# Kernel optimization log

Measured on AMD Instinct MI355X. Metric: run time of the kernel, lower is better.

## Reference

```python
import jax, jax.numpy as jnp
import numpy as np

B, S, D_MODEL, N_HEADS, MAX_LEN = 2, 1024, 1024, 16, 1024
D_K = D_MODEL // N_HEADS


def setup_inputs() -> dict:
    key = jax.random.key(0)
    ks = jax.random.split(key, 8)
    w_std = 1.0 / np.sqrt(D_MODEL)  # ~ torch Linear default scale
    inp = {
        "query": jax.random.normal(ks[0], (B, S, D_MODEL), jnp.float32),
        "key": jax.random.normal(ks[1], (B, S, D_MODEL), jnp.float32),
        "value": jax.random.normal(ks[2], (B, S, D_MODEL), jnp.float32),
        "Wq": jax.random.normal(ks[3], (D_MODEL, D_MODEL), jnp.float32) * w_std,
        "Wk": jax.random.normal(ks[4], (D_MODEL, D_MODEL), jnp.float32) * w_std,
        "Wv": jax.random.normal(ks[5], (D_MODEL, D_MODEL), jnp.float32) * w_std,
        "Wo": jax.random.normal(ks[6], (D_MODEL, D_MODEL), jnp.float32) * w_std,
        "bq": jnp.zeros((D_MODEL,), jnp.float32),
        "bk": jnp.zeros((D_MODEL,), jnp.float32),
        "bv": jnp.zeros((D_MODEL,), jnp.float32),
        "bo": jnp.zeros((D_MODEL,), jnp.float32),
        "Er": jax.random.normal(ks[7], (2 * MAX_LEN - 1, D_K), jnp.float32) * 0.02,
    }
    return inp


def _rel_positions(q_len, k_len, max_len):
    pos = jnp.arange(q_len)[:, None] - jnp.arange(k_len)[None, :]
    pos = jnp.clip(pos, -max_len + 1, max_len - 1)
    return pos + max_len - 1  # [q_len, k_len] indices into Er


def reference(query, key, value, Wq, Wk, Wv, Wo, bq, bk, bv, bo, Er):
    b, q_len, d_model = query.shape
    k_len = key.shape[1]
    d_k = Er.shape[-1]
    h = d_model // d_k
    scale = 1.0 / np.sqrt(d_k)

    def proj(x, W, bias):  # torch Linear: x @ W.T + b, then split heads -> [b,h,s,d_k]
        y = x @ W.T + bias
        return y.reshape(b, -1, h, d_k).transpose(0, 2, 1, 3)

    q = proj(query, Wq, bq)
    k = proj(key, Wk, bk)
    v = proj(value, Wv, bv)

    positions = _rel_positions(q_len, k_len, MAX_LEN)  # [q,k]
    # QEr[b,h,q,k] = sum_d q[b,h,q,d] * Er[positions[q,k], d]
    # computed as a full contraction against Er then a gather on the relative axis
    qe_all = jnp.einsum('bhqd,rd->bhqr', q, Er)  # [b,h,q,2*max_len-1]
    qer = jnp.take_along_axis(qe_all, positions[None, None, :, :], axis=-1)  # [b,h,q,k]

    qk = jnp.einsum('bhqd,bhkd->bhqk', q, k)
    scores = (qk + qer) * scale
    p_attn = jax.nn.softmax(scores, axis=-1)  # dropout=0.0 (eval)
    out = jnp.einsum('bhqk,bhkd->bhqd', p_attn, v)

    out = out.transpose(0, 2, 1, 3).reshape(b, q_len, h * d_k)
    return out @ Wo.T + bo
```

## Files before the change

kernel.cpp:

```cpp
#include <hip/hip_runtime.h>
#include <hip/hip_bf16.h>
#include <cstdint>
#include <cstddef>

typedef __attribute__((ext_vector_type(8))) short bf16x8;
typedef __attribute__((ext_vector_type(4))) float f32x4;
typedef unsigned short u16;
typedef unsigned int u32;

#define DEV static __device__ __forceinline__

constexpr int Sc = 1024, DMc = 1024, Hc = 16, DKc = 64;

DEV u16 f2bf(float f) {
  u32 u = __float_as_uint(f);
  return (u16)((u + 0x7FFFu + ((u >> 16) & 1u)) >> 16);
}
DEV float bf2f(u16 h) { return __uint_as_float(((u32)h) << 16); }

#define GLDS16(g, l)                                                        \
  __builtin_amdgcn_global_load_lds(                                         \
      (const __attribute__((address_space(1))) void*)(g),                   \
      (__attribute__((address_space(3))) void*)(l), 16, 0, 0)

struct CvtJob { const float* in; u16* out; int nchunk; int rsh; int nreal; };
struct CvtArgs { CvtJob j[8]; };

__global__ __launch_bounds__(256) void cvt_kernel(CvtArgs a) {
  CvtJob job = a.j[blockIdx.y];
  int ci = (int)(blockIdx.x * 256 + threadIdx.x);
  if (ci >= job.nchunk) return;
  bf16x8 o = {};
  if (ci < job.nreal) {
    const float* src = job.in + (size_t)ci * 8;
    float4 v0 = *(const float4*)src;
    float4 v1 = *(const float4*)(src + 4);
    o[0] = (short)f2bf(v0.x); o[1] = (short)f2bf(v0.y);
    o[2] = (short)f2bf(v0.z); o[3] = (short)f2bf(v0.w);
    o[4] = (short)f2bf(v1.x); o[5] = (short)f2bf(v1.y);
    o[6] = (short)f2bf(v1.z); o[7] = (short)f2bf(v1.w);
  }
  int row = ci >> job.rsh;
  int co = (ci & ~7) | ((ci & 7) ^ (row & 7));
  *(bf16x8*)(job.out + (size_t)co * 8) = o;
}

struct GemmJob { const u16* A; const u16* W; const float* bias; void* out; };
struct GemmArgs { GemmJob p[3]; };

template<int BM, int MODE>
__global__ __launch_bounds__(256, 2) void gemm_bt(GemmArgs G) {
  constexpr int MI = BM / 32;
  __shared__ __align__(16) u16 sA[2][BM * 64];
  __shared__ __align__(16) u16 sB[2][128 * 64];
  const int tid = threadIdx.x, lane = tid & 63, w = tid >> 6;
  const int cl = lane & 15, rg = lane >> 4;
  const int srow = lane >> 3, schk = lane & 7;
  int z, m0, n0;
  if (MODE == 0) {
    int id = blockIdx.x;
    if (id < 512) { z = id >> 8; int r = id & 255; m0 = (r >> 3) * 64; n0 = (r & 7) * 128; }
    else          { z = 2;       int r = id - 512; m0 = (r >> 4) * 64; n0 = (r & 15) * 128; }
  } else {
    z = 0; int id = blockIdx.x; m0 = (id >> 3) * 64; n0 = (id & 7) * 128;
  }
  GemmJob P = G.p[z];
  constexpr int K = 1024;
  const int wm = (w >> 1) * (MI * 16), wn = (w & 1) * 64;
  f32x4 acc[MI][4] = {};

  auto stage = [&](int kt, int b) {
    const u16* Ab = P.A + (size_t)m0 * K + kt * 64;
    const u16* Wb = P.W + (size_t)n0 * K + kt * 64;
    #pragma unroll
    for (int i = 0; i < BM / 32; ++i)
      GLDS16(Ab + (size_t)(i * 32 + w * 8 + srow) * K + schk * 8, &sA[b][(i * 32 + w * 8) * 64]);
    #pragma unroll
    for (int i = 0; i < 4; ++i)
      GLDS16(Wb + (size_t)(i * 32 + w * 8 + srow) * K + schk * 8, &sB[b][(i * 32 + w * 8) * 64]);
  };

  stage(0, 0);
  for (int kt = 0; kt < 16; ++kt) {
    __syncthreads();
    if (kt < 15) stage(kt + 1, (kt + 1) & 1);
    const u16* A_ = sA[kt & 1];
    const u16* B_ = sB[kt & 1];
    #pragma unroll
    for (int kk = 0; kk < 2; ++kk) {
      bf16x8 af[MI], bfr[4];
      #pragma unroll
      for (int mi = 0; mi < MI; ++mi) {
        int row = wm + mi * 16 + cl;
        af[mi] = *(const bf16x8*)(A_ + row * 64 + ((kk * 4 + rg) ^ (row & 7)) * 8);
      }
      #pragma unroll
      for (int ni = 0; ni < 4; ++ni) {
        int row = wn + ni * 16 + cl;
        bfr[ni] = *(const bf16x8*)(B_ + row * 64 + ((kk * 4 + rg) ^ (row & 7)) * 8);
      }
      #pragma unroll
      for (int mi = 0; mi < MI; ++mi)
        #pragma unroll
        for (int ni = 0; ni < 4; ++ni)
          acc[mi][ni] = __builtin_amdgcn_mfma_f32_16x16x32_bf16(af[mi], bfr[ni], acc[mi][ni], 0, 0, 0);
    }
  }
  #pragma unroll
  for (int mi = 0; mi < MI; ++mi) {
    #pragma unroll
    for (int ni = 0; ni < 4; ++ni) {
      #pragma unroll
      for (int j = 0; j < 4; ++j) {
        int m = m0 + wm + mi * 16 + rg * 4 + j;
        int n = n0 + wn + ni * 16 + cl;
        if (MODE == 1) {
          ((float*)P.out)[(size_t)m * DMc + n] = acc[mi][ni][j] + P.bias[n];
        } else if (z < 2) {
          float v = acc[mi][ni][j] + P.bias[n];
          int h = n >> 6, d = n & 63;
          int c2 = (d >> 3) ^ (m & 7);
          ((u16*)P.out)[((size_t)((m >> 10) * Hc + h) * Sc + (m & 1023)) * DKc + c2 * 8 + (d & 7)] = f2bf(v);
        } else {
          float v = acc[mi][ni][j] + P.bias[m];
          int d = m & 63, h = m >> 6, bb = n >> 10, s = n & 1023;
          int c2 = ((s & 63) >> 3) ^ (d & 7);
          ((u16*)P.out)[((size_t)(bb * Hc + h) * DKc + d) * Sc + (s & ~63) + c2 * 8 + (s & 7)] = f2bf(v);
        }
      }
    }
  }
}

__global__ __launch_bounds__(256, 4) void attn_rel(
    const u16* __restrict__ qg, const u16* __restrict__ kg,
    const u16* __restrict__ vtg, const u16* __restrict__ erg,
    u16* __restrict__ Opart, float* __restrict__ lpart) {
  __shared__ __align__(16) u16 sK[64 * 64];
  __shared__ __align__(16) u16 sV[64 * 64];
  __shared__ __align__(16) u16 sU[4][1440];
  const int tid = threadIdx.x, lane = tid & 63, w = tid >> 6;
  const int cl = lane & 15, rg = lane >> 4;
  const int key = cl & 7;
  const int bh = blockIdx.x & 31, qt = (blockIdx.x >> 5) & 15, half = blockIdx.x >> 9;
  const int q0 = qt * 64, t0 = half * 8;

  const u16* qrow = qg + ((size_t)bh * Sc + q0 + w * 16 + cl) * DKc;
  bf16x8 qf0 = *(const bf16x8*)(qrow + (rg ^ key) * 8);
  bf16x8 qf1 = *(const bf16x8*)(qrow + ((rg + 4) ^ key) * 8);
  f32x4 oacc[4] = {};
  float lsum = 0.f;
  u16* Uw = sU[w];
  const u16* kbase = kg + (size_t)bh * Sc * DKc;
  const u16* vbase = vtg + (size_t)bh * DKc * Sc;

  auto stage = [&](int t) {
    const u16* ks = kbase + t * 64 * 64;
    #pragma unroll
    for (int i = 0; i < 2; ++i) {
      GLDS16(ks + (i * 32 + w * 8) * 64 + lane * 8, &sK[(i * 32 + w * 8) * 64]);
      GLDS16(vbase + (size_t)(i * 32 + w * 8 + (lane >> 3)) * Sc + t * 64 + (lane & 7) * 8,
             &sV[(i * 32 + w * 8) * 64]);
    }
  };

  stage(t0);
  for (int tt = 0; tt < 8; ++tt) {
    const int t = t0 + tt;
    __syncthreads();

    f32x4 sct[4];
    #pragma unroll
    for (int nc = 0; nc < 4; ++nc) {
      const u16* kr = sK + (nc * 16 + cl) * 64;
      bf16x8 b0 = *(const bf16x8*)(kr + (rg ^ key) * 8);
      bf16x8 b1 = *(const bf16x8*)(kr + ((rg + 4) ^ key) * 8);
      f32x4 a = {};
      a = __builtin_amdgcn_mfma_f32_16x16x32_bf16(b0, qf0, a, 0, 0, 0);
      a = __builtin_amdgcn_mfma_f32_16x16x32_bf16(b1, qf1, a, 0, 0, 0);
      sct[nc] = a;
    }
    const u16* ebase = erg + (size_t)(q0 + w * 16 - t * 64 + 960) * DKc;
    #pragma unroll
    for (int rc0 = 0; rc0 < 5; ++rc0) {
      const u16* er = ebase + (size_t)(rc0 * 16 + cl) * DKc;
      bf16x8 e0 = *(const bf16x8*)(er + (rg ^ key) * 8);
      bf16x8 e1 = *(const bf16x8*)(er + ((rg + 4) ^ key) * 8);
      f32x4 a = {};
      a = __builtin_amdgcn_mfma_f32_16x16x32_bf16(qf0, e0, a, 0, 0, 0);
      a = __builtin_amdgcn_mfma_f32_16x16x32_bf16(qf1, e1, a, 0, 0, 0);
      u16* tp = Uw + (rc0 * 16 + cl) * 18 + rg * 4;
      ushort2 lo, hi;
      lo.x = f2bf(a[0]); lo.y = f2bf(a[1]);
      hi.x = f2bf(a[2]); hi.y = f2bf(a[3]);
      *(ushort2*)tp = lo;
      *(ushort2*)(tp + 2) = hi;
    }
    float pv[4][4];
    #pragma unroll
    for (int nc = 0; nc < 4; ++nc) {
      #pragma unroll
      for (int j = 0; j < 4; ++j) {
        int r = cl + 63 - (nc * 16 + rg * 4 + j);
        float tval = bf2f(Uw[r * 18 + cl]);
        float p = __expf((sct[nc][j] + tval) * 0.125f);
        lsum += p;
        pv[nc][j] = p;
      }
    }
    #pragma unroll
    for (int nc = 0; nc < 4; ++nc) {
      ushort4 pk;
      pk.x = f2bf(pv[nc][0]); pk.y = f2bf(pv[nc][1]);
      pk.z = f2bf(pv[nc][2]); pk.w = f2bf(pv[nc][3]);
      *(ushort4*)(Uw + cl * 76 + nc * 16 + rg * 4) = pk;
    }
    bf16x8 pa0 = *(const bf16x8*)(Uw + cl * 76 + rg * 8);
    bf16x8 pa1 = *(const bf16x8*)(Uw + cl * 76 + 32 + rg * 8);
    #pragma unroll
    for (int dc = 0; dc < 4; ++dc) {
      const u16* vr = sV + (dc * 16 + cl) * 64;
      bf16x8 b0 = *(const bf16x8*)(vr + (rg ^ key) * 8);
      bf16x8 b1 = *(const bf16x8*)(vr + ((rg + 4) ^ key) * 8);
      oacc[dc] = __builtin_amdgcn_mfma_f32_16x16x32_bf16(pa0, b0, oacc[dc], 0, 0, 0);
      oacc[dc] = __builtin_amdgcn_mfma_f32_16x16x32_bf16(pa1, b1, oacc[dc], 0, 0, 0);
    }
    __syncthreads();
    if (tt < 7) stage(t + 1);
  }
  lsum += __shfl_xor(lsum, 16);
  lsum += __shfl_xor(lsum, 32);
  const size_t pb = (size_t)(half * 32 + bh) * Sc;
  if (rg == 0) lpart[pb + q0 + w * 16 + cl] = lsum;
  u16* Ob = Opart + (pb + q0 + w * 16) * DKc;
  #pragma unroll
  for (int dc = 0; dc < 4; ++dc)
    #pragma unroll
    for (int j = 0; j < 4; ++j)
      Ob[(rg * 4 + j) * DKc + dc * 16 + cl] = f2bf(oacc[dc][j]);
}

__global__ __launch_bounds__(256) void merge_kernel(
    const u16* __restrict__ O, const float* __restrict__ l,
    u16* __restrict__ attnb) {
  int ci = (int)(blockIdx.x * 256 + threadIdx.x);
  int bh = ci >> 13, rem = ci & 8191, s = rem >> 3, dc = rem & 7;
  const u16* o0 = O + ((size_t)bh * Sc + s) * DKc + dc * 8;
  const u16* o1 = o0 + (size_t)32 * Sc * DKc;
  float rinv = 1.0f / (l[(size_t)bh * Sc + s] + l[(size_t)(32 + bh) * Sc + s]);
  bf16x8 a = *(const bf16x8*)o0;
  bf16x8 b = *(const bf16x8*)o1;
  bf16x8 o;
  #pragma unroll
  for (int e = 0; e < 8; ++e)
    o[e] = (short)f2bf((bf2f((u16)a[e]) + bf2f((u16)b[e])) * rinv);
  int bb = bh >> 4, h = bh & 15;
  int c2 = dc ^ (s & 7);
  *(bf16x8*)(attnb + ((size_t)(bb * Sc + s)) * DMc + h * DKc + c2 * 8) = o;
}

extern "C" void kernel_launch(void* const* d_in, const int* in_sizes, int n_in,
                              void* d_out, int out_size, void* d_ws, size_t ws_size,
                              hipStream_t stream) {
  (void)in_sizes; (void)n_in; (void)out_size; (void)ws_size;
  const float* query = (const float*)d_in[0];
  const float* key_  = (const float*)d_in[1];
  const float* value = (const float*)d_in[2];
  const float* Wq = (const float*)d_in[3];
  const float* Wk = (const float*)d_in[4];
  const float* Wv = (const float*)d_in[5];
  const float* Wo = (const float*)d_in[6];
  const float* bq = (const float*)d_in[7];
  const float* bk = (const float*)d_in[8];
  const float* bv = (const float*)d_in[9];
  const float* bo = (const float*)d_in[10];
  const float* Er = (const float*)d_in[11];

  char* p = (char*)d_ws;
  size_t off = 0;
  auto alloc = [&](size_t bytes) {
    char* r = p + off;
    off += (bytes + 255) & ~(size_t)255;
    return r;
  };
  u16* Xq  = (u16*)alloc((size_t)2048 * 1024 * 2);
  u16* Xk  = (u16*)alloc((size_t)2048 * 1024 * 2);
  u16* Xv  = (u16*)alloc((size_t)2048 * 1024 * 2);
  u16* Wqb = (u16*)alloc((size_t)1024 * 1024 * 2);
  u16* Wkb = (u16*)alloc((size_t)1024 * 1024 * 2);
  u16* Wvb = (u16*)alloc((size_t)1024 * 1024 * 2);
  u16* Wob = (u16*)alloc((size_t)1024 * 1024 * 2);
  u16* Erb = (u16*)alloc((size_t)2048 * 64 * 2);
  u16* qh  = (u16*)alloc((size_t)2048 * 1024 * 2);
  u16* kh  = (u16*)alloc((size_t)2048 * 1024 * 2);
  u16* vt  = (u16*)alloc((size_t)2048 * 1024 * 2);
  u16* attnb = (u16*)alloc((size_t)2048 * 1024 * 2);
  u16* Opart = (u16*)alloc((size_t)2 * 32 * 1024 * 64 * 2);
  float* lpart = (float*)alloc((size_t)2 * 32 * 1024 * 4);

  CvtArgs ca;
  ca.j[0] = {query, Xq, 262144, 7, 262144};
  ca.j[1] = {key_,  Xk, 262144, 7, 262144};
  ca.j[2] = {value, Xv, 262144, 7, 262144};
  ca.j[3] = {Wq, Wqb, 131072, 7, 131072};
  ca.j[4] = {Wk, Wkb, 131072, 7, 131072};
  ca.j[5] = {Wv, Wvb, 131072, 7, 131072};
  ca.j[6] = {Wo, Wob, 131072, 7, 131072};
  ca.j[7] = {Er, Erb, 16384, 3, 16376};
  cvt_kernel<<<dim3(1024, 8, 1), 256, 0, stream>>>(ca);

  GemmArgs gp;
  gp.p[0] = {Xq, Wqb, bq, (void*)qh};
  gp.p[1] = {Xk, Wkb, bk, (void*)kh};
  gp.p[2] = {Wvb, Xv, bv, (void*)vt};
  gemm_bt<64, 0><<<dim3(768, 1, 1), 256, 0, stream>>>(gp);

  attn_rel<<<dim3(1024, 1, 1), 256, 0, stream>>>(qh, kh, vt, Erb, Opart, lpart);

  merge_kernel<<<dim3(1024, 1, 1), 256, 0, stream>>>(Opart, lpart, attnb);

  GemmArgs go;
  go.p[0] = {attnb, Wob, bo, d_out};
  go.p[1] = go.p[0];
  go.p[2] = go.p[0];
  gemm_bt<64, 1><<<dim3(256, 1, 1), 256, 0, stream>>>(go);
}
```

Baseline: 96.20 us.

## Fuse activation fp32-to-bf16 conversion and split-merge into GEMM operand loading

```diff
diff --git a/kernel.cpp b/kernel.cpp
--- a/kernel.cpp
+++ b/kernel.cpp
@@ -18,13 +18,19 @@
 }
 DEV float bf2f(u16 h) { return __uint_as_float(((u32)h) << 16); }
 
+DEV u32 cvtpk(float a, float b) {
+  u32 r;
+  asm("v_cvt_pk_bf16_f32 %0, %1, %2" : "=v"(r) : "v"(a), "v"(b));
+  return r;
+}
+
 #define GLDS16(g, l)                                                        \
   __builtin_amdgcn_global_load_lds(                                         \
       (const __attribute__((address_space(1))) void*)(g),                   \
       (__attribute__((address_space(3))) void*)(l), 16, 0, 0)
 
 struct CvtJob { const float* in; u16* out; int nchunk; int rsh; int nreal; };
-struct CvtArgs { CvtJob j[8]; };
+struct CvtArgs { CvtJob j[5]; };
 
 __global__ __launch_bounds__(256) void cvt_kernel(CvtArgs a) {
   CvtJob job = a.j[blockIdx.y];
@@ -45,78 +51,136 @@
   *(bf16x8*)(job.out + (size_t)co * 8) = o;
 }
 
-struct GemmJob { const u16* A; const u16* W; const float* bias; void* out; };
-struct GemmArgs { GemmJob p[3]; };
-
-template<int BM, int MODE>
+struct GemmJob { const void* A; const void* W; const float* bias; void* out; const float* aux; };
+struct GemmArgs { GemmJob p[2]; };
+
+template<int BM, int BN, int MODE>
 __global__ __launch_bounds__(256, 2) void gemm_bt(GemmArgs G) {
-  constexpr int MI = BM / 32;
+  constexpr int MI = BM / 32, NI = BN / 32;
   __shared__ __align__(16) u16 sA[2][BM * 64];
-  __shared__ __align__(16) u16 sB[2][128 * 64];
+  __shared__ __align__(16) u16 sB[2][BN * 64];
   const int tid = threadIdx.x, lane = tid & 63, w = tid >> 6;
   const int cl = lane & 15, rg = lane >> 4;
   const int srow = lane >> 3, schk = lane & 7;
   int z, m0, n0;
-  if (MODE == 0) {
-    int id = blockIdx.x;
-    if (id < 512) { z = id >> 8; int r = id & 255; m0 = (r >> 3) * 64; n0 = (r & 7) * 128; }
-    else          { z = 2;       int r = id - 512; m0 = (r >> 4) * 64; n0 = (r & 15) * 128; }
-  } else {
-    z = 0; int id = blockIdx.x; m0 = (id >> 3) * 64; n0 = (id & 7) * 128;
-  }
+  if (MODE == 0)      { int id = blockIdx.x; z = id >> 8; int r = id & 255; m0 = (r >> 3) * 64; n0 = (r & 7) * 128; }
+  else if (MODE == 2) { int id = blockIdx.x; z = 0; m0 = (id >> 5) * 64; n0 = (id & 31) * 64; }
+  else                { int id = blockIdx.x; z = 0; m0 = (id >> 4) * 64; n0 = (id & 15) * 64; }
   GemmJob P = G.p[z];
-  constexpr int K = 1024;
-  const int wm = (w >> 1) * (MI * 16), wn = (w & 1) * 64;
-  f32x4 acc[MI][4] = {};
-
-  auto stage = [&](int kt, int b) {
-    const u16* Ab = P.A + (size_t)m0 * K + kt * 64;
-    const u16* Wb = P.W + (size_t)n0 * K + kt * 64;
-    #pragma unroll
-    for (int i = 0; i < BM / 32; ++i)
-      GLDS16(Ab + (size_t)(i * 32 + w * 8 + srow) * K + schk * 8, &sA[b][(i * 32 + w * 8) * 64]);
-    #pragma unroll
-    for (int i = 0; i < 4; ++i)
-      GLDS16(Wb + (size_t)(i * 32 + w * 8 + srow) * K + schk * 8, &sB[b][(i * 32 + w * 8) * 64]);
+  const int wm = (w >> 1) * (BM / 2), wn = (w & 1) * (BN / 2);
+  f32x4 acc[MI][NI] = {};
+
+  float4 fa[2][2];
+  bf16x8 ma[2][2];
+  float  ml[2][2];
+
+  auto issue = [&](int kt, int b) {
+    if (MODE == 0) {
+      #pragma unroll
+      for (int i = 0; i < 2; ++i) {
+        int ch = i * 256 + tid, row = ch >> 3, c = ch & 7;
+        const float* src = (const float*)P.A + (size_t)(m0 + row) * 1024 + kt * 64 + c * 8;
+        fa[i][0] = *(const float4*)src;
+        fa[i][1] = *(const float4*)(src + 4);
+      }
+      #pragma unroll
+      for (int i = 0; i < 4; ++i)
+        GLDS16((const u16*)P.W + (size_t)(n0 + i * 32 + w * 8 + srow) * 1024 + kt * 64 + schk * 8,
+               &sB[b][(i * 32 + w * 8) * 64]);
+    } else if (MODE == 2) {
+      #pragma unroll
+      for (int i = 0; i < 2; ++i) {
+        int ch = i * 256 + tid, row = ch >> 3, c = ch & 7;
+        const float* src = (const float*)P.W + (size_t)(n0 + row) * 1024 + kt * 64 + c * 8;
+        fa[i][0] = *(const float4*)src;
+        fa[i][1] = *(const float4*)(src + 4);
+      }
+      #pragma unroll
+      for (int i = 0; i < 2; ++i)
+        GLDS16((const u16*)P.A + (size_t)(m0 + i * 32 + w * 8 + srow) * 1024 + kt * 64 + schk * 8,
+               &sA[b][(i * 32 + w * 8) * 64]);
+    } else {
+      #pragma unroll
+      for (int i = 0; i < 2; ++i) {
+        int ch = i * 256 + tid, row = ch >> 3, c = ch & 7;
+        int rgl = m0 + row, bb = rgl >> 10, s = rgl & 1023;
+        const u16* o0 = (const u16*)P.A + ((size_t)(bb * 16 + kt) * 1024 + s) * 64 + c * 8;
+        ma[i][0] = *(const bf16x8*)o0;
+        ma[i][1] = *(const bf16x8*)(o0 + (size_t)32 * 1024 * 64);
+        ml[i][0] = P.aux[(size_t)(bb * 16 + kt) * 1024 + s];
+        ml[i][1] = P.aux[(size_t)(32 + bb * 16 + kt) * 1024 + s];
+      }
+      #pragma unroll
+      for (int i = 0; i < 2; ++i)
+        GLDS16((const u16*)P.W + (size_t)(n0 + i * 32 + w * 8 + srow) * 1024 + kt * 64 + schk * 8,
+               &sB[b][(i * 32 + w * 8) * 64]);
+    }
   };
 
-  stage(0, 0);
+  auto commit = [&](int b) {
+    #pragma unroll
+    for (int i = 0; i < 2; ++i) {
+      int ch = i * 256 + tid, row = ch >> 3, c = ch & 7;
+      uint4 v4;
+      if (MODE == 0 || MODE == 2) {
+        v4.x = cvtpk(fa[i][0].x, fa[i][0].y);
+        v4.y = cvtpk(fa[i][0].z, fa[i][0].w);
+        v4.z = cvtpk(fa[i][1].x, fa[i][1].y);
+        v4.w = cvtpk(fa[i][1].z, fa[i][1].w);
+      } else {
+        float rinv = 1.0f / (ml[i][0] + ml[i][1]);
+        u32 pk[4];
+        #pragma unroll
+        for (int p = 0; p < 4; ++p) {
+          float v0 = (bf2f((u16)ma[i][0][2 * p])     + bf2f((u16)ma[i][1][2 * p]))     * rinv;
+          float v1 = (bf2f((u16)ma[i][0][2 * p + 1]) + bf2f((u16)ma[i][1][2 * p + 1])) * rinv;
+          pk[p] = cvtpk(v0, v1);
+        }
+        v4.x = pk[0]; v4.y = pk[1]; v4.z = pk[2]; v4.w = pk[3];
+      }
+      u16* dst = (MODE == 2) ? sB[b] : sA[b];
+      *(uint4*)(dst + row * 64 + (c ^ (row & 7)) * 8) = v4;
+    }
+  };
+
+  issue(0, 0);
+  commit(0);
   for (int kt = 0; kt < 16; ++kt) {
     __syncthreads();
-    if (kt < 15) stage(kt + 1, (kt + 1) & 1);
-    const u16* A_ = sA[kt & 1];
-    const u16* B_ = sB[kt & 1];
+    const int b = kt & 1;
+    if (kt < 15) issue(kt + 1, b ^ 1);
     #pragma unroll
     for (int kk = 0; kk < 2; ++kk) {
-      bf16x8 af[MI], bfr[4];
+      bf16x8 af[MI], bfr[NI];
       #pragma unroll
       for (int mi = 0; mi < MI; ++mi) {
         int row = wm + mi * 16 + cl;
-        af[mi] = *(const bf16x8*)(A_ + row * 64 + ((kk * 4 + rg) ^ (row & 7)) * 8);
-      }
-      #pragma unroll
-      for (int ni = 0; ni < 4; ++ni) {
+        af[mi] = *(const bf16x8*)(sA[b] + row * 64 + ((kk * 4 + rg) ^ (row & 7)) * 8);
+      }
+      #pragma unroll
+      for (int ni = 0; ni < NI; ++ni) {
         int row = wn + ni * 16 + cl;
-        bfr[ni] = *(const bf16x8*)(B_ + row * 64 + ((kk * 4 + rg) ^ (row & 7)) * 8);
+        bfr[ni] = *(const bf16x8*)(sB[b] + row * 64 + ((kk * 4 + rg) ^ (row & 7)) * 8);
       }
       #pragma unroll
       for (int mi = 0; mi < MI; ++mi)
         #pragma unroll
-        for (int ni = 0; ni < 4; ++ni)
+        for (int ni = 0; ni < NI; ++ni)
           acc[mi][ni] = __builtin_amdgcn_mfma_f32_16x16x32_bf16(af[mi], bfr[ni], acc[mi][ni], 0, 0, 0);
     }
+    if (kt < 15) commit(b ^ 1);
   }
   #pragma unroll
   for (int mi = 0; mi < MI; ++mi) {
     #pragma unroll
-    for (int ni = 0; ni < 4; ++ni) {
+    for (int ni = 0; ni < NI; ++ni) {
       #pragma unroll
       for (int j = 0; j < 4; ++j) {
         int m = m0 + wm + mi * 16 + rg * 4 + j;
         int n = n0 + wn + ni * 16 + cl;
         if (MODE == 1) {
           ((float*)P.out)[(size_t)m * DMc + n] = acc[mi][ni][j] + P.bias[n];
-        } else if (z < 2) {
+        } else if (MODE == 0) {
           float v = acc[mi][ni][j] + P.bias[n];
           int h = n >> 6, d = n & 63;
           int c2 = (d >> 3) ^ (m & 7);
@@ -196,6 +260,8 @@
       *(ushort2*)tp = lo;
       *(ushort2*)(tp + 2) = hi;
     }
+    asm volatile("s_waitcnt lgkmcnt(0)" ::: "memory");
+    __builtin_amdgcn_sched_barrier(0);
     float pv[4][4];
     #pragma unroll
     for (int nc = 0; nc < 4; ++nc) {
@@ -215,6 +281,8 @@
       pk.z = f2bf(pv[nc][2]); pk.w = f2bf(pv[nc][3]);
       *(ushort4*)(Uw + cl * 76 + nc * 16 + rg * 4) = pk;
     }
+    asm volatile("s_waitcnt lgkmcnt(0)" ::: "memory");
+    __builtin_amdgcn_sched_barrier(0);
     bf16x8 pa0 = *(const bf16x8*)(Uw + cl * 76 + rg * 8);
     bf16x8 pa1 = *(const bf16x8*)(Uw + cl * 76 + 32 + rg * 8);
     #pragma unroll
@@ -238,25 +306,6 @@
     #pragma unroll
     for (int j = 0; j < 4; ++j)
       Ob[(rg * 4 + j) * DKc + dc * 16 + cl] = f2bf(oacc[dc][j]);
-}
-
-__global__ __launch_bounds__(256) void merge_kernel(
-    const u16* __restrict__ O, const float* __restrict__ l,
-    u16* __restrict__ attnb) {
-  int ci = (int)(blockIdx.x * 256 + threadIdx.x);
-  int bh = ci >> 13, rem = ci & 8191, s = rem >> 3, dc = rem & 7;
-  const u16* o0 = O + ((size_t)bh * Sc + s) * DKc + dc * 8;
-  const u16* o1 = o0 + (size_t)32 * Sc * DKc;
-  float rinv = 1.0f / (l[(size_t)bh * Sc + s] + l[(size_t)(32 + bh) * Sc + s]);
-  bf16x8 a = *(const bf16x8*)o0;
-  bf16x8 b = *(const bf16x8*)o1;
-  bf16x8 o;
-  #pragma unroll
-  for (int e = 0; e < 8; ++e)
-    o[e] = (short)f2bf((bf2f((u16)a[e]) + bf2f((u16)b[e])) * rinv);
-  int bb = bh >> 4, h = bh & 15;
-  int c2 = dc ^ (s & 7);
-  *(bf16x8*)(attnb + ((size_t)(bb * Sc + s)) * DMc + h * DKc + c2 * 8) = o;
 }
 
 extern "C" void kernel_launch(void* const* d_in, const int* in_sizes, int n_in,
@@ -283,9 +332,6 @@
     off += (bytes + 255) & ~(size_t)255;
     return r;
   };
-  u16* Xq  = (u16*)alloc((size_t)2048 * 1024 * 2);
-  u16* Xk  = (u16*)alloc((size_t)2048 * 1024 * 2);
-  u16* Xv  = (u16*)alloc((size_t)2048 * 1024 * 2);
   u16* Wqb = (u16*)alloc((size_t)1024 * 1024 * 2);
   u16* Wkb = (u16*)alloc((size_t)1024 * 1024 * 2);
   u16* Wvb = (u16*)alloc((size_t)1024 * 1024 * 2);
@@ -294,34 +340,31 @@
   u16* qh  = (u16*)alloc((size_t)2048 * 1024 * 2);
   u16* kh  = (u16*)alloc((size_t)2048 * 1024 * 2);
   u16* vt  = (u16*)alloc((size_t)2048 * 1024 * 2);
-  u16* attnb = (u16*)alloc((size_t)2048 * 1024 * 2);
   u16* Opart = (u16*)alloc((size_t)2 * 32 * 1024 * 64 * 2);
   float* lpart = (float*)alloc((size_t)2 * 32 * 1024 * 4);
 
   CvtArgs ca;
-  ca.j[0] = {query, Xq, 262144, 7, 262144};
-  ca.j[1] = {key_,  Xk, 262144, 7, 262144};
-  ca.j[2] = {value, Xv, 262144, 7, 262144};
-  ca.j[3] = {Wq, Wqb, 131072, 7, 131072};
-  ca.j[4] = {Wk, Wkb, 131072, 7, 131072};
-  ca.j[5] = {Wv, Wvb, 131072, 7, 131072};
-  ca.j[6] = {Wo, Wob, 131072, 7, 131072};
-  ca.j[7] = {Er, Erb, 16384, 3, 16376};
-  cvt_kernel<<<dim3(1024, 8, 1), 256, 0, stream>>>(ca);
-
-  GemmArgs gp;
-  gp.p[0] = {Xq, Wqb, bq, (void*)qh};
-  gp.p[1] = {Xk, Wkb, bk, (void*)kh};
-  gp.p[2] = {Wvb, Xv, bv, (void*)vt};
-  gemm_bt<64, 0><<<dim3(768, 1, 1), 256, 0, stream>>>(gp);
+  ca.j[0] = {Wq, Wqb, 131072, 7, 131072};
+  ca.j[1] = {Wk, Wkb, 131072, 7, 131072};
+  ca.j[2] = {Wv, Wvb, 131072, 7, 131072};
+  ca.j[3] = {Wo, Wob, 131072, 7, 131072};
+  ca.j[4] = {Er, Erb, 16384, 3, 16376};
+  cvt_kernel<<<dim3(512, 5, 1), 256, 0, stream>>>(ca);
+
+  GemmArgs gqk;
+  gqk.p[0] = {query, Wqb, bq, (void*)qh, nullptr};
+  gqk.p[1] = {key_,  Wkb, bk, (void*)kh, nullptr};
+  gemm_bt<64, 128, 0><<<dim3(512, 1, 1), 256, 0, stream>>>(gqk);
+
+  GemmArgs gv;
+  gv.p[0] = {Wvb, value, bv, (void*)vt, nullptr};
+  gv.p[1] = gv.p[0];
+  gemm_bt<64, 64, 2><<<dim3(512, 1, 1), 256, 0, stream>>>(gv);
 
   attn_rel<<<dim3(1024, 1, 1), 256, 0, stream>>>(qh, kh, vt, Erb, Opart, lpart);
 
-  merge_kernel<<<dim3(1024, 1, 1), 256, 0, stream>>>(Opart, lpart, attnb);
-
   GemmArgs go;
-  go.p[0] = {attnb, Wob, bo, d_out};
+  go.p[0] = {Opart, Wob, bo, d_out, lpart};
   go.p[1] = go.p[0];
-  go.p[2] = go.p[0];
-  gemm_bt<64, 1><<<dim3(256, 1, 1), 256, 0, stream>>>(go);
-}
+  gemm_bt<64, 64, 1><<<dim3(512, 1, 1), 256, 0, stream>>>(go);
+}
```

New measurement: 104.2 us. 8.3% more time.
